# Performance work log

Hardware: AMD Instinct MI355X
Metric: run time of the kernel (lower is better)

Reference implementation:

```python
import jax, jax.numpy as jnp
import numpy as np

EPS = 1e-5
MAX_NORM = 1.0 - 1e-5  # clamp for atanh / ball projection


def mob_add(u, v):
    # Mobius addition on each d_ball (last dim), c=1
    uv = jnp.sum(u * v, axis=-1, keepdims=True)
    uu = jnp.sum(u * u, axis=-1, keepdims=True)
    vv = jnp.sum(v * v, axis=-1, keepdims=True)
    num = (1.0 + 2.0 * uv + vv) * u + (1.0 - uu) * v
    den = 1.0 + 2.0 * uv + uu * vv
    return num / jnp.maximum(den, EPS)


def log_map_zero(y):
    # log map at origin, per ball (last dim)
    n = jnp.linalg.norm(y, axis=-1, keepdims=True)
    n_c = jnp.clip(n, EPS, MAX_NORM)
    return jnp.arctanh(n_c) * y / n_c


def mob_mat_mul_d(W, x, d):
    # W: (n_in, d, n_out, d); x: (B, n_in, d) -> (B, n_out, d)
    # Mobius matvec on the flattened product-ball representation.
    B = x.shape[0]
    x_f = x.reshape(B, -1)                      # (B, n_in*d)
    W_f = W.reshape(x_f.shape[-1], -1)          # (n_in*d, n_out*d)
    Mx = x_f @ W_f                              # (B, n_out*d)
    x_n = jnp.clip(jnp.linalg.norm(x_f, axis=-1, keepdims=True), EPS, MAX_NORM)
    Mx_n = jnp.maximum(jnp.linalg.norm(Mx, axis=-1, keepdims=True), EPS)
    res = jnp.tanh(Mx_n / x_n * jnp.arctanh(x_n)) * (Mx / Mx_n)
    return res.reshape(B, -1, d)


def mob_pointwise_prod(x, u):
    # diagonal Mobius scaling of hyperbolic x by euclidean gate u, per ball
    ux = u * x
    x_n = jnp.clip(jnp.linalg.norm(x, axis=-1, keepdims=True), EPS, MAX_NORM)
    ux_n = jnp.maximum(jnp.linalg.norm(ux, axis=-1, keepdims=True), EPS)
    return jnp.tanh(ux_n / x_n * jnp.arctanh(x_n)) * (ux / ux_n)


def transition(W, h, U, x, b, d):
    Wh = mob_mat_mul_d(W, h, d)
    Ux = mob_mat_mul_d(U, x, d)
    return mob_add(mob_add(Wh, Ux), b)


def setup_inputs() -> dict:
    key = jax.random.key(0)
    ks = jax.random.split(key, 8)
    B, I, H, D = 16384, 256, 256, 4
    k = (1.0 / H) ** 0.5
    # scale points to lie strictly inside the Poincare ball
    hyp_x = 0.02 * jax.random.normal(ks[0], (B, I, D), dtype=jnp.float32)
    hidden = 0.02 * jax.random.normal(ks[1], (B, H, D), dtype=jnp.float32)
    mk = lambda kk, n_in: jax.random.uniform(kk, (n_in, D, H, D), minval=-k, maxval=k, dtype=jnp.float32)
    return dict(
        hyp_x=hyp_x, hidden=hidden,
        w_z=mk(ks[2], H), w_r=mk(ks[3], H), w_h=mk(ks[4], H),
        u_z=mk(ks[5], I), u_r=mk(ks[6], I), u_h=mk(ks[7], I),
        b_z=jnp.zeros((H, D), jnp.float32),
        b_r=jnp.zeros((H, D), jnp.float32),
        b_h=jnp.zeros((H, D), jnp.float32),
    )


def reference(hyp_x, hidden, w_z, w_r, w_h, u_z, u_r, u_h, b_z, b_r, b_h):
    d = hyp_x.shape[-1]
    z = jax.nn.sigmoid(log_map_zero(transition(w_z, hidden, u_z, hyp_x, b_z, d)))
    r = jax.nn.sigmoid(log_map_zero(transition(w_r, hidden, u_r, hyp_x, b_r, d)))
    r_point_h = mob_pointwise_prod(hidden, r)
    # NOTE: original code uses u_r here (not u_h) -- kept faithful
    h_tilde = transition(w_h, r_point_h, u_r, hyp_x, b_h, d)
    minus_h_oplus_htilde = mob_add(-hidden, h_tilde)
    new_h = mob_add(hidden, mob_pointwise_prod(minus_h_oplus_htilde, z))
    return new_h
```

## Files before the change

### kernel.cpp

```cpp
#include <hip/hip_runtime.h>
#include <stdint.h>

#define EPSF 1e-5f
#define MAXNF (1.0f - 1e-5f)

typedef __attribute__((ext_vector_type(8))) short short8;
typedef __attribute__((ext_vector_type(4))) float floatx4;

__device__ __forceinline__ unsigned short f2bf(float f){
  union { float f; uint32_t u; } v; v.f = f;
  return (unsigned short)((v.u + 0x7FFFu + ((v.u >> 16) & 1u)) >> 16);
}
__device__ __forceinline__ float bf2f(unsigned short s){
  union { uint32_t u; float f; } v; v.u = ((uint32_t)s) << 16;
  return v.f;
}
__device__ __forceinline__ float4 bf2f4(ushort4 s){
  return make_float4(bf2f(s.x), bf2f(s.y), bf2f(s.z), bf2f(s.w));
}
__device__ __forceinline__ uint32_t cvtpk(float lo, float hi){
  uint32_t r; asm("v_cvt_pk_bf16_f32 %0, %1, %2" : "=v"(r) : "v"(lo), "v"(hi));
  return r;
}
__device__ __forceinline__ void store_bf4(unsigned short* p, float4 v){
  uint2 r; r.x = cvtpk(v.x, v.y); r.y = cvtpk(v.z, v.w);
  *(uint2*)p = r;
}
__device__ __forceinline__ float fsqrt(float x){ return __builtin_amdgcn_sqrtf(x); }

__device__ __forceinline__ void gload16(const void* g, void* l){
  __builtin_amdgcn_global_load_lds(
      (__attribute__((address_space(1))) void*)(uintptr_t)g,
      (__attribute__((address_space(3))) void*)l, 16, 0, 0);
}

__device__ __forceinline__ float fatanh(float x){
  return 0.5f * __logf(__fdividef(1.f + x, 1.f - x));
}
__device__ __forceinline__ float ftanh_pos(float x){
  const float t = __expf(-2.f * x);
  return __fdividef(1.f - t, 1.f + t);
}
__device__ __forceinline__ float fsig(float x){
  return __fdividef(1.f, 1.f + __expf(-x));
}

__global__ __launch_bounds__(256, 4) void cast_norm_k(const float* __restrict__ X,
                                                      unsigned short* __restrict__ Xbf,
                                                      float* __restrict__ nrm){
  const int row = blockIdx.x, t = threadIdx.x;
  const float4 v = ((const float4*)(X + (size_t)row*1024))[t];
  store_bf4(Xbf + (size_t)row*1024 + 4*t, v);
  float ss = v.x*v.x + v.y*v.y + v.z*v.z + v.w*v.w;
  #pragma unroll
  for (int o = 32; o; o >>= 1) ss += __shfl_down(ss, o);
  __shared__ float red[4];
  const int lane = t & 63, w = t >> 6;
  if (lane == 0) red[w] = ss;
  __syncthreads();
  if (t == 0) nrm[row] = fsqrt(red[0] + red[1] + red[2] + red[3]);
}

__global__ void wcast_k(const float* __restrict__ W, unsigned short* __restrict__ Wt){
  __shared__ float tile[32][33];
  const int tx = threadIdx.x, ty = threadIdx.y;
  const int k0 = blockIdx.x * 32, n0 = blockIdx.y * 32;
  #pragma unroll
  for (int i = 0; i < 4; ++i)
    tile[ty + i*8][tx] = W[(size_t)(k0 + ty + i*8) * 1024 + n0 + tx];
  __syncthreads();
  #pragma unroll
  for (int i = 0; i < 4; ++i)
    Wt[(size_t)(n0 + ty + i*8) * 1024 + k0 + tx] = f2bf(tile[tx][ty + i*8]);
}

#define GBM 128
#define GBN 256
#define GBK 32
#define GKD 1024

__global__ __launch_bounds__(512) void gemm_k(const unsigned short* __restrict__ A,
                                              const unsigned short* __restrict__ Bt,
                                              unsigned short* __restrict__ C,
                                              int lda, int ldc){
  __shared__ unsigned short smem[2*4096 + 2*8192];
  unsigned short* As = smem;
  unsigned short* Bs = smem + 2*4096;
  const int tid = threadIdx.x;
  const int lane = tid & 63, w = tid >> 6;
  const int wr = w >> 2, wc = w & 3;
  const int lr = lane & 15, kg = lane >> 4;
  const int row0 = blockIdx.y * GBM, col0 = blockIdx.x * GBN;

  int aoff[4], boff[4];
  #pragma unroll
  for (int a = 0; a < 4; ++a){
    const int r = wr*64 + a*16 + lr;
    aoff[a] = r*32 + ((kg ^ (r & 3)) << 3);
  }
  #pragma unroll
  for (int b = 0; b < 4; ++b){
    const int r = wc*64 + b*16 + lr;
    boff[b] = r*32 + ((kg ^ (r & 3)) << 3);
  }

  floatx4 acc[4][4] = {};

  auto stage = [&](int buf, int kt){
    {
      const int flat = tid;
      const int r = flat >> 2, cp = flat & 3, c = cp ^ (r & 3);
      gload16(A + (size_t)(row0 + r)*lda + kt*GBK + c*8, As + buf*4096 + flat*8);
    }
    #pragma unroll
    for (int i = 0; i < 2; ++i){
      const int flat = i*512 + tid;
      const int r = flat >> 2, cp = flat & 3, c = cp ^ (r & 3);
      gload16(Bt + (size_t)(col0 + r)*GKD + kt*GBK + c*8, Bs + buf*8192 + flat*8);
    }
  };

  stage(0, 0);
  __syncthreads();
  int cur = 0;
  for (int kt = 0; kt < GKD/GBK; ++kt){
    if (kt + 1 < GKD/GBK) stage(cur ^ 1, kt + 1);
    const unsigned short* as = As + cur*4096;
    const unsigned short* bs = Bs + cur*8192;
    short8 af[4], bfv[4];
    #pragma unroll
    for (int a = 0; a < 4; ++a) af[a] = *(const short8*)(as + aoff[a]);
    #pragma unroll
    for (int b = 0; b < 4; ++b) bfv[b] = *(const short8*)(bs + boff[b]);
    #pragma unroll
    for (int a = 0; a < 4; ++a)
      #pragma unroll
      for (int b = 0; b < 4; ++b)
        acc[a][b] = __builtin_amdgcn_mfma_f32_16x16x32_bf16(af[a], bfv[b], acc[a][b], 0, 0, 0);
    __syncthreads();
    cur ^= 1;
  }

  const int crow0 = row0 + wr*64;
  const int ccol = col0 + wc*64 + lr;
  #pragma unroll
  for (int a = 0; a < 4; ++a){
    #pragma unroll
    for (int j = 0; j < 4; ++j){
      const int r = crow0 + a*16 + kg*4 + j;
      unsigned short* cp = C + (size_t)r*ldc + ccol;
      #pragma unroll
      for (int b = 0; b < 4; ++b) cp[b*16] = f2bf(acc[a][b][j]);
    }
  }
}

__device__ __forceinline__ float dot4(const float4 a, const float4 b){
  return a.x*b.x + a.y*b.y + a.z*b.z + a.w*b.w;
}
__device__ __forceinline__ float4 scal4(const float4 a, float s){
  return make_float4(a.x*s, a.y*s, a.z*s, a.w*s);
}
__device__ __forceinline__ float clipn(float n){ return fminf(fmaxf(n, EPSF), MAXNF); }

__device__ __forceinline__ float4 mob_add4(const float4 u, const float4 v){
  const float uv = dot4(u,v), uu = dot4(u,u), vv = dot4(v,v);
  const float cu = 1.f + 2.f*uv + vv, cv = 1.f - uu;
  const float inv = __fdividef(1.f, fmaxf(1.f + 2.f*uv + uu*vv, EPSF));
  return make_float4((cu*u.x + cv*v.x)*inv, (cu*u.y + cv*v.y)*inv,
                     (cu*u.z + cv*v.z)*inv, (cu*u.w + cv*v.w)*inv);
}

__device__ __forceinline__ float4 logmap_sig4(const float4 y){
  const float n = fsqrt(dot4(y,y));
  const float nc = clipn(n);
  const float s = __fdividef(fatanh(nc), nc);
  return make_float4(fsig(s*y.x), fsig(s*y.y), fsig(s*y.z), fsig(s*y.w));
}

__device__ __forceinline__ float4 mob_pp4(const float4 x, const float4 u){
  const float4 ux = make_float4(u.x*x.x, u.y*x.y, u.z*x.z, u.w*x.w);
  const float xn = clipn(fsqrt(dot4(x,x)));
  const float uxn = fmaxf(fsqrt(dot4(ux,ux)), EPSF);
  const float s = __fdividef(ftanh_pos(__fdividef(uxn, xn) * fatanh(xn)), uxn);
  return scal4(ux, s);
}

__global__ __launch_bounds__(256, 4) void epi1_k(unsigned short* C1, unsigned short* C2,
                       const float* hidden, const float* bz, const float* br,
                       const float* h_nrm, const float* x_nrm, float* rph_nrm){
  const int row = blockIdx.x, t = threadIdx.x;
  const int lane = t & 63, w = t >> 6;
  const size_t b2 = (size_t)row*2048;
  const float4 mzh  = bf2f4(((const ushort4*)(C1 + b2))[t]);
  const float4 mrh4 = bf2f4(((const ushort4*)(C1 + b2))[256 + t]);
  const float4 mzx4 = bf2f4(((const ushort4*)(C2 + b2))[t]);
  const float4 mrx4 = bf2f4(((const ushort4*)(C2 + b2))[256 + t]);
  float s0 = dot4(mzh,mzh), s1 = dot4(mzx4,mzx4), s2 = dot4(mrh4,mrh4), s3 = dot4(mrx4,mrx4);
  #pragma unroll
  for (int o = 32; o; o >>= 1){
    s0 += __shfl_down(s0,o); s1 += __shfl_down(s1,o);
    s2 += __shfl_down(s2,o); s3 += __shfl_down(s3,o);
  }
  __shared__ float red[4][4];
  if (lane == 0){ red[w][0]=s0; red[w][1]=s1; red[w][2]=s2; red[w][3]=s3; }
  __syncthreads();
  const float nMzh = fmaxf(fsqrt(red[0][0]+red[1][0]+red[2][0]+red[3][0]), EPSF);
  const float nMzx = fmaxf(fsqrt(red[0][1]+red[1][1]+red[2][1]+red[3][1]), EPSF);
  const float nMrh = fmaxf(fsqrt(red[0][2]+red[1][2]+red[2][2]+red[3][2]), EPSF);
  const float nMrx = fmaxf(fsqrt(red[0][3]+red[1][3]+red[2][3]+red[3][3]), EPSF);
  const float hnc = clipn(h_nrm[row]), xnc = clipn(x_nrm[row]);
  const float atH = fatanh(hnc), atX = fatanh(xnc);
  const float swz = __fdividef(ftanh_pos(__fdividef(nMzh, hnc)*atH), nMzh);
  const float suz = __fdividef(ftanh_pos(__fdividef(nMzx, xnc)*atX), nMzx);
  const float swr = __fdividef(ftanh_pos(__fdividef(nMrh, hnc)*atH), nMrh);
  const float sur = __fdividef(ftanh_pos(__fdividef(nMrx, xnc)*atX), nMrx);
  const float4 bz4 = ((const float4*)bz)[t];
  const float4 br4 = ((const float4*)br)[t];
  const float4 z4 = logmap_sig4(mob_add4(mob_add4(scal4(mzh,swz), scal4(mzx4,suz)), bz4));
  const float4 UxR = scal4(mrx4, sur);
  const float4 r4 = logmap_sig4(mob_add4(mob_add4(scal4(mrh4,swr), UxR), br4));
  store_bf4(C1 + b2 + 4*t, z4);
  store_bf4(C1 + b2 + 1024 + 4*t, UxR);
  const float4 h4 = ((const float4*)(hidden + (size_t)row*1024))[t];
  const float4 rph = mob_pp4(h4, r4);
  store_bf4(C2 + b2 + 4*t, rph);
  float sr = dot4(rph, rph);
  #pragma unroll
  for (int o = 32; o; o >>= 1) sr += __shfl_down(sr,o);
  __syncthreads();
  if (lane == 0) red[w][0] = sr;
  __syncthreads();
  if (t == 0) rph_nrm[row] = fsqrt(red[0][0]+red[1][0]+red[2][0]+red[3][0]);
}

__global__ __launch_bounds__(256, 4) void epi2_k(const unsigned short* mh,
                       const unsigned short* C1,
                       const float* hidden, const float* bh,
                       const float* rph_nrm, float* __restrict__ out){
  const int row = blockIdx.x, t = threadIdx.x;
  const int lane = t & 63, w = t >> 6;
  const size_t base = (size_t)row*1024, b2 = (size_t)row*2048;
  const float4 mh4 = bf2f4(((const ushort4*)(mh + base))[t]);
  float ss = dot4(mh4, mh4);
  #pragma unroll
  for (int o = 32; o; o >>= 1) ss += __shfl_down(ss,o);
  __shared__ float red[4];
  if (lane == 0) red[w] = ss;
  __syncthreads();
  const float nMh = fmaxf(fsqrt(red[0]+red[1]+red[2]+red[3]), EPSF);
  const float rnc = clipn(rph_nrm[row]);
  const float swh = __fdividef(ftanh_pos(__fdividef(nMh, rnc)*fatanh(rnc)), nMh);
  const float4 WhH = scal4(mh4, swh);
  const float4 Ux4 = bf2f4(((const ushort4*)(C1 + b2))[256 + t]);
  const float4 bh4 = ((const float4*)bh)[t];
  const float4 ht = mob_add4(mob_add4(WhH, Ux4), bh4);
  const float4 h4 = ((const float4*)(hidden + base))[t];
  const float4 nh4 = make_float4(-h4.x, -h4.y, -h4.z, -h4.w);
  const float4 m4 = mob_add4(nh4, ht);
  const float4 z4 = bf2f4(((const ushort4*)(C1 + b2))[t]);
  const float4 p4 = mob_pp4(m4, z4);
  const float4 o4 = mob_add4(h4, p4);
  ((float4*)(out + base))[t] = o4;
}

extern "C" void kernel_launch(void* const* d_in, const int* in_sizes, int n_in,
                              void* d_out, int out_size, void* d_ws, size_t ws_size,
                              hipStream_t stream) {
  (void)in_sizes; (void)n_in; (void)out_size; (void)ws_size;
  const float* hyp_x  = (const float*)d_in[0];
  const float* hidden = (const float*)d_in[1];
  const float* w_z = (const float*)d_in[2];
  const float* w_r = (const float*)d_in[3];
  const float* w_h = (const float*)d_in[4];
  const float* u_z = (const float*)d_in[5];
  const float* u_r = (const float*)d_in[6];
  const float* b_z = (const float*)d_in[8];
  const float* b_r = (const float*)d_in[9];
  const float* b_h = (const float*)d_in[10];
  float* out = (float*)d_out;

  const size_t NROW = 16384, MAT = NROW*1024;
  unsigned short* hbf = (unsigned short*)d_ws;
  unsigned short* xbf = hbf + MAT;
  unsigned short* C1  = xbf + MAT;
  unsigned short* wzr = C1 + 2*MAT;
  unsigned short* uzr = wzr + 2*1048576;
  unsigned short* wht = uzr + 2*1048576;
  float* h_n   = (float*)(wht + 1048576);
  float* x_n   = h_n + NROW;
  float* rph_n = x_n + NROW;
  unsigned short* C2 = (unsigned short*)d_out;

  cast_norm_k<<<dim3(16384), dim3(256), 0, stream>>>(hidden, hbf, h_n);
  cast_norm_k<<<dim3(16384), dim3(256), 0, stream>>>(hyp_x, xbf, x_n);

  dim3 wg(32, 32), wb(32, 8);
  wcast_k<<<wg, wb, 0, stream>>>(w_z, wzr);
  wcast_k<<<wg, wb, 0, stream>>>(w_r, wzr + 1048576);
  wcast_k<<<wg, wb, 0, stream>>>(u_z, uzr);
  wcast_k<<<wg, wb, 0, stream>>>(u_r, uzr + 1048576);
  wcast_k<<<wg, wb, 0, stream>>>(w_h, wht);

  gemm_k<<<dim3(8,128), dim3(512), 0, stream>>>(hbf, wzr, C1, 1024, 2048);
  gemm_k<<<dim3(8,128), dim3(512), 0, stream>>>(xbf, uzr, C2, 1024, 2048);

  epi1_k<<<dim3(16384), dim3(256), 0, stream>>>(C1, C2, hidden, b_z, b_r,
                                                h_n, x_n, rph_n);

  gemm_k<<<dim3(4,128), dim3(512), 0, stream>>>(C2 , wht,
                                                hbf , 2048, 1024);

  epi2_k<<<dim3(16384), dim3(256), 0, stream>>>(hbf, C1, hidden, b_h, rph_n, out);
}
```

Baseline: 374.6 us.

## Map one row per wavefront in row kernels and read hidden from bf16 copy

The cast and epilogue kernels now process one row per 64-lane wavefront, four rows per block, using xor-shuffle reductions in place of shared-memory reductions and block barriers. The epilogues read the bf16 copy of hidden instead of the fp32 input, which halves that traffic at some precision cost. The third GEMM now writes into the spare half of C2 rather than overwriting hbf, so hbf stays valid for the second epilogue. The aim is to cut barrier and launch overhead and memory traffic in the bandwidth-bound elementwise stages, in exchange for lower-precision hidden values in the epilogue math.

Result: faster. 347.4 us (-7.2%).

```diff
diff --git a/kernel.cpp b/kernel.cpp
--- a/kernel.cpp
+++ b/kernel.cpp
@@ -11,22 +11,26 @@
   union { float f; uint32_t u; } v; v.f = f;
   return (unsigned short)((v.u + 0x7FFFu + ((v.u >> 16) & 1u)) >> 16);
 }
-__device__ __forceinline__ float bf2f(unsigned short s){
-  union { uint32_t u; float f; } v; v.u = ((uint32_t)s) << 16;
-  return v.f;
-}
-__device__ __forceinline__ float4 bf2f4(ushort4 s){
-  return make_float4(bf2f(s.x), bf2f(s.y), bf2f(s.z), bf2f(s.w));
+__device__ __forceinline__ float bf_lo(uint32_t u){
+  union { uint32_t u; float f; } v; v.u = u << 16; return v.f;
+}
+__device__ __forceinline__ float bf_hi(uint32_t u){
+  union { uint32_t u; float f; } v; v.u = u & 0xffff0000u; return v.f;
 }
 __device__ __forceinline__ uint32_t cvtpk(float lo, float hi){
   uint32_t r; asm("v_cvt_pk_bf16_f32 %0, %1, %2" : "=v"(r) : "v"(lo), "v"(hi));
   return r;
 }
-__device__ __forceinline__ void store_bf4(unsigned short* p, float4 v){
-  uint2 r; r.x = cvtpk(v.x, v.y); r.y = cvtpk(v.z, v.w);
-  *(uint2*)p = r;
-}
 __device__ __forceinline__ float fsqrt(float x){ return __builtin_amdgcn_sqrtf(x); }
+
+__device__ __forceinline__ float4 ld_ball(const unsigned short* rowp, int b){
+  const uint2 u = *(const uint2*)(rowp + 4*b);
+  return make_float4(bf_lo(u.x), bf_hi(u.x), bf_lo(u.y), bf_hi(u.y));
+}
+__device__ __forceinline__ void st_ball(unsigned short* rowp, int b, float4 f){
+  uint2 u; u.x = cvtpk(f.x, f.y); u.y = cvtpk(f.z, f.w);
+  *(uint2*)(rowp + 4*b) = u;
+}
 
 __device__ __forceinline__ void gload16(const void* g, void* l){
   __builtin_amdgcn_global_load_lds(
@@ -45,20 +49,56 @@
   return __fdividef(1.f, 1.f + __expf(-x));
 }
 
-__global__ __launch_bounds__(256, 4) void cast_norm_k(const float* __restrict__ X,
-                                                      unsigned short* __restrict__ Xbf,
-                                                      float* __restrict__ nrm){
-  const int row = blockIdx.x, t = threadIdx.x;
-  const float4 v = ((const float4*)(X + (size_t)row*1024))[t];
-  store_bf4(Xbf + (size_t)row*1024 + 4*t, v);
-  float ss = v.x*v.x + v.y*v.y + v.z*v.z + v.w*v.w;
-  #pragma unroll
-  for (int o = 32; o; o >>= 1) ss += __shfl_down(ss, o);
-  __shared__ float red[4];
-  const int lane = t & 63, w = t >> 6;
-  if (lane == 0) red[w] = ss;
-  __syncthreads();
-  if (t == 0) nrm[row] = fsqrt(red[0] + red[1] + red[2] + red[3]);
+__device__ __forceinline__ float wsum(float v){
+  #pragma unroll
+  for (int o = 32; o; o >>= 1) v += __shfl_xor(v, o);
+  return v;
+}
+
+__device__ __forceinline__ float dot4(const float4 a, const float4 b){
+  return a.x*b.x + a.y*b.y + a.z*b.z + a.w*b.w;
+}
+__device__ __forceinline__ float4 scal4(const float4 a, float s){
+  return make_float4(a.x*s, a.y*s, a.z*s, a.w*s);
+}
+__device__ __forceinline__ float clipn(float n){ return fminf(fmaxf(n, EPSF), MAXNF); }
+
+__device__ __forceinline__ float4 mob_add4(const float4 u, const float4 v){
+  const float uv = dot4(u,v), uu = dot4(u,u), vv = dot4(v,v);
+  const float cu = 1.f + 2.f*uv + vv, cv = 1.f - uu;
+  const float inv = __fdividef(1.f, fmaxf(1.f + 2.f*uv + uu*vv, EPSF));
+  return make_float4((cu*u.x + cv*v.x)*inv, (cu*u.y + cv*v.y)*inv,
+                     (cu*u.z + cv*v.z)*inv, (cu*u.w + cv*v.w)*inv);
+}
+__device__ __forceinline__ float4 logmap_sig4(const float4 y){
+  const float nc = clipn(fsqrt(dot4(y,y)));
+  const float s = __fdividef(fatanh(nc), nc);
+  return make_float4(fsig(s*y.x), fsig(s*y.y), fsig(s*y.z), fsig(s*y.w));
+}
+__device__ __forceinline__ float4 mob_pp4(const float4 x, const float4 u){
+  const float4 ux = make_float4(u.x*x.x, u.y*x.y, u.z*x.z, u.w*x.w);
+  const float xn = clipn(fsqrt(dot4(x,x)));
+  const float uxn = fmaxf(fsqrt(dot4(ux,ux)), EPSF);
+  const float s = __fdividef(ftanh_pos(__fdividef(uxn, xn) * fatanh(xn)), uxn);
+  return scal4(ux, s);
+}
+
+__global__ void cast_norm_k(const float* __restrict__ X, unsigned short* __restrict__ Xbf,
+                            float* __restrict__ nrm){
+  const int lane = threadIdx.x & 63;
+  const int row  = blockIdx.x*4 + (threadIdx.x >> 6);
+  const float4* xr = (const float4*)(X + (size_t)row*1024);
+  unsigned short* br_ = Xbf + (size_t)row*1024;
+  float ss = 0.f;
+  #pragma unroll
+  for (int i = 0; i < 4; ++i){
+    const int b = lane + 64*i;
+    const float4 v = xr[b];
+    st_ball(br_, b, v);
+    ss += dot4(v, v);
+  }
+  ss = wsum(ss);
+  if (lane == 0) nrm[row] = fsqrt(ss);
 }
 
 __global__ void wcast_k(const float* __restrict__ W, unsigned short* __restrict__ Wt){
@@ -155,113 +195,99 @@
   }
 }
 
-__device__ __forceinline__ float dot4(const float4 a, const float4 b){
-  return a.x*b.x + a.y*b.y + a.z*b.z + a.w*b.w;
-}
-__device__ __forceinline__ float4 scal4(const float4 a, float s){
-  return make_float4(a.x*s, a.y*s, a.z*s, a.w*s);
-}
-__device__ __forceinline__ float clipn(float n){ return fminf(fmaxf(n, EPSF), MAXNF); }
-
-__device__ __forceinline__ float4 mob_add4(const float4 u, const float4 v){
-  const float uv = dot4(u,v), uu = dot4(u,u), vv = dot4(v,v);
-  const float cu = 1.f + 2.f*uv + vv, cv = 1.f - uu;
-  const float inv = __fdividef(1.f, fmaxf(1.f + 2.f*uv + uu*vv, EPSF));
-  return make_float4((cu*u.x + cv*v.x)*inv, (cu*u.y + cv*v.y)*inv,
-                     (cu*u.z + cv*v.z)*inv, (cu*u.w + cv*v.w)*inv);
-}
-
-__device__ __forceinline__ float4 logmap_sig4(const float4 y){
-  const float n = fsqrt(dot4(y,y));
-  const float nc = clipn(n);
-  const float s = __fdividef(fatanh(nc), nc);
-  return make_float4(fsig(s*y.x), fsig(s*y.y), fsig(s*y.z), fsig(s*y.w));
-}
-
-__device__ __forceinline__ float4 mob_pp4(const float4 x, const float4 u){
-  const float4 ux = make_float4(u.x*x.x, u.y*x.y, u.z*x.z, u.w*x.w);
-  const float xn = clipn(fsqrt(dot4(x,x)));
-  const float uxn = fmaxf(fsqrt(dot4(ux,ux)), EPSF);
-  const float s = __fdividef(ftanh_pos(__fdividef(uxn, xn) * fatanh(xn)), uxn);
-  return scal4(ux, s);
-}
-
-__global__ __launch_bounds__(256, 4) void epi1_k(unsigned short* C1, unsigned short* C2,
-                       const float* hidden, const float* bz, const float* br,
-                       const float* h_nrm, const float* x_nrm, float* rph_nrm){
-  const int row = blockIdx.x, t = threadIdx.x;
-  const int lane = t & 63, w = t >> 6;
-  const size_t b2 = (size_t)row*2048;
-  const float4 mzh  = bf2f4(((const ushort4*)(C1 + b2))[t]);
-  const float4 mrh4 = bf2f4(((const ushort4*)(C1 + b2))[256 + t]);
-  const float4 mzx4 = bf2f4(((const ushort4*)(C2 + b2))[t]);
-  const float4 mrx4 = bf2f4(((const ushort4*)(C2 + b2))[256 + t]);
-  float s0 = dot4(mzh,mzh), s1 = dot4(mzx4,mzx4), s2 = dot4(mrh4,mrh4), s3 = dot4(mrx4,mrx4);
-  #pragma unroll
-  for (int o = 32; o; o >>= 1){
-    s0 += __shfl_down(s0,o); s1 += __shfl_down(s1,o);
-    s2 += __shfl_down(s2,o); s3 += __shfl_down(s3,o);
-  }
-  __shared__ float red[4][4];
-  if (lane == 0){ red[w][0]=s0; red[w][1]=s1; red[w][2]=s2; red[w][3]=s3; }
-  __syncthreads();
-  const float nMzh = fmaxf(fsqrt(red[0][0]+red[1][0]+red[2][0]+red[3][0]), EPSF);
-  const float nMzx = fmaxf(fsqrt(red[0][1]+red[1][1]+red[2][1]+red[3][1]), EPSF);
-  const float nMrh = fmaxf(fsqrt(red[0][2]+red[1][2]+red[2][2]+red[3][2]), EPSF);
-  const float nMrx = fmaxf(fsqrt(red[0][3]+red[1][3]+red[2][3]+red[3][3]), EPSF);
+__global__ __launch_bounds__(256) __attribute__((amdgpu_waves_per_eu(4,4)))
+void epi1_k(unsigned short* C1, unsigned short* C2, const unsigned short* hbf,
+            const float* bz, const float* br,
+            const float* h_nrm, const float* x_nrm, float* rph_nrm){
+  const int lane = threadIdx.x & 63;
+  const int row  = blockIdx.x*4 + (threadIdx.x >> 6);
+  unsigned short* c1lo = C1 + (size_t)row*2048;
+  unsigned short* c1hi = c1lo + 1024;
+  unsigned short* c2lo = C2 + (size_t)row*2048;
+  unsigned short* c2hi = c2lo + 1024;
+  const unsigned short* hr = hbf + (size_t)row*1024;
+
+  float4 mzh[4], mrh[4], mzx[4], mrx[4];
+  float s0 = 0.f, s1 = 0.f, s2 = 0.f, s3 = 0.f;
+  #pragma unroll
+  for (int i = 0; i < 4; ++i){
+    const int b = lane + 64*i;
+    mzh[i] = ld_ball(c1lo, b); mrh[i] = ld_ball(c1hi, b);
+    mzx[i] = ld_ball(c2lo, b); mrx[i] = ld_ball(c2hi, b);
+    s0 += dot4(mzh[i], mzh[i]); s1 += dot4(mzx[i], mzx[i]);
+    s2 += dot4(mrh[i], mrh[i]); s3 += dot4(mrx[i], mrx[i]);
+  }
+  s0 = wsum(s0); s1 = wsum(s1); s2 = wsum(s2); s3 = wsum(s3);
+
+  const float nMzh = fmaxf(fsqrt(s0), EPSF);
+  const float nMzx = fmaxf(fsqrt(s1), EPSF);
+  const float nMrh = fmaxf(fsqrt(s2), EPSF);
+  const float nMrx = fmaxf(fsqrt(s3), EPSF);
   const float hnc = clipn(h_nrm[row]), xnc = clipn(x_nrm[row]);
   const float atH = fatanh(hnc), atX = fatanh(xnc);
   const float swz = __fdividef(ftanh_pos(__fdividef(nMzh, hnc)*atH), nMzh);
   const float suz = __fdividef(ftanh_pos(__fdividef(nMzx, xnc)*atX), nMzx);
   const float swr = __fdividef(ftanh_pos(__fdividef(nMrh, hnc)*atH), nMrh);
   const float sur = __fdividef(ftanh_pos(__fdividef(nMrx, xnc)*atX), nMrx);
-  const float4 bz4 = ((const float4*)bz)[t];
-  const float4 br4 = ((const float4*)br)[t];
-  const float4 z4 = logmap_sig4(mob_add4(mob_add4(scal4(mzh,swz), scal4(mzx4,suz)), bz4));
-  const float4 UxR = scal4(mrx4, sur);
-  const float4 r4 = logmap_sig4(mob_add4(mob_add4(scal4(mrh4,swr), UxR), br4));
-  store_bf4(C1 + b2 + 4*t, z4);
-  store_bf4(C1 + b2 + 1024 + 4*t, UxR);
-  const float4 h4 = ((const float4*)(hidden + (size_t)row*1024))[t];
-  const float4 rph = mob_pp4(h4, r4);
-  store_bf4(C2 + b2 + 4*t, rph);
-  float sr = dot4(rph, rph);
-  #pragma unroll
-  for (int o = 32; o; o >>= 1) sr += __shfl_down(sr,o);
-  __syncthreads();
-  if (lane == 0) red[w][0] = sr;
-  __syncthreads();
-  if (t == 0) rph_nrm[row] = fsqrt(red[0][0]+red[1][0]+red[2][0]+red[3][0]);
-}
-
-__global__ __launch_bounds__(256, 4) void epi2_k(const unsigned short* mh,
-                       const unsigned short* C1,
-                       const float* hidden, const float* bh,
-                       const float* rph_nrm, float* __restrict__ out){
-  const int row = blockIdx.x, t = threadIdx.x;
-  const int lane = t & 63, w = t >> 6;
-  const size_t base = (size_t)row*1024, b2 = (size_t)row*2048;
-  const float4 mh4 = bf2f4(((const ushort4*)(mh + base))[t]);
-  float ss = dot4(mh4, mh4);
-  #pragma unroll
-  for (int o = 32; o; o >>= 1) ss += __shfl_down(ss,o);
-  __shared__ float red[4];
-  if (lane == 0) red[w] = ss;
-  __syncthreads();
-  const float nMh = fmaxf(fsqrt(red[0]+red[1]+red[2]+red[3]), EPSF);
+
+  float sr = 0.f;
+  #pragma unroll
+  for (int i = 0; i < 4; ++i){
+    const int b = lane + 64*i;
+    const float4 bz4 = ((const float4*)bz)[b];
+    const float4 br4 = ((const float4*)br)[b];
+    const float4 z4  = logmap_sig4(mob_add4(mob_add4(scal4(mzh[i],swz), scal4(mzx[i],suz)), bz4));
+    const float4 UxR = scal4(mrx[i], sur);
+    const float4 r4  = logmap_sig4(mob_add4(mob_add4(scal4(mrh[i],swr), UxR), br4));
+    st_ball(c1lo, b, z4);
+    st_ball(c1hi, b, UxR);
+    const float4 h4  = ld_ball(hr, b);
+    const float4 rph = mob_pp4(h4, r4);
+    st_ball(c2lo, b, rph);
+    sr += dot4(rph, rph);
+  }
+  sr = wsum(sr);
+  if (lane == 0) rph_nrm[row] = fsqrt(sr);
+}
+
+__global__ __launch_bounds__(256) __attribute__((amdgpu_waves_per_eu(4,4)))
+void epi2_k(const unsigned short* C1, const unsigned short* C2,
+            const unsigned short* hbf, const float* bh,
+            const float* rph_nrm, float* out){
+  const int lane = threadIdx.x & 63;
+  const int row  = blockIdx.x*4 + (threadIdx.x >> 6);
+  const unsigned short* c1lo = C1 + (size_t)row*2048;
+  const unsigned short* c1hi = c1lo + 1024;
+  const unsigned short* c2hi = C2 + (size_t)row*2048 + 1024;
+  const unsigned short* hr = hbf + (size_t)row*1024;
+  float4* outr = (float4*)(out + (size_t)row*1024);
+
+  float4 mh[4];
+  float ss = 0.f;
+  #pragma unroll
+  for (int i = 0; i < 4; ++i){
+    mh[i] = ld_ball(c2hi, lane + 64*i);
+    ss += dot4(mh[i], mh[i]);
+  }
+  ss = wsum(ss);
+  const float nMh = fmaxf(fsqrt(ss), EPSF);
   const float rnc = clipn(rph_nrm[row]);
   const float swh = __fdividef(ftanh_pos(__fdividef(nMh, rnc)*fatanh(rnc)), nMh);
-  const float4 WhH = scal4(mh4, swh);
-  const float4 Ux4 = bf2f4(((const ushort4*)(C1 + b2))[256 + t]);
-  const float4 bh4 = ((const float4*)bh)[t];
-  const float4 ht = mob_add4(mob_add4(WhH, Ux4), bh4);
-  const float4 h4 = ((const float4*)(hidden + base))[t];
-  const float4 nh4 = make_float4(-h4.x, -h4.y, -h4.z, -h4.w);
-  const float4 m4 = mob_add4(nh4, ht);
-  const float4 z4 = bf2f4(((const ushort4*)(C1 + b2))[t]);
-  const float4 p4 = mob_pp4(m4, z4);
-  const float4 o4 = mob_add4(h4, p4);
-  ((float4*)(out + base))[t] = o4;
+
+  #pragma unroll
+  for (int i = 0; i < 4; ++i){
+    const int b = lane + 64*i;
+    const float4 WhH = scal4(mh[i], swh);
+    const float4 Ux4 = ld_ball(c1hi, b);
+    const float4 bh4 = ((const float4*)bh)[b];
+    const float4 ht  = mob_add4(mob_add4(WhH, Ux4), bh4);
+    const float4 h4  = ld_ball(hr, b);
+    const float4 nh4 = make_float4(-h4.x, -h4.y, -h4.z, -h4.w);
+    const float4 m4  = mob_add4(nh4, ht);
+    const float4 z4  = ld_ball(c1lo, b);
+    const float4 p4  = mob_pp4(m4, z4);
+    outr[b] = mob_add4(h4, p4);
+  }
 }
 
 extern "C" void kernel_launch(void* const* d_in, const int* in_sizes, int n_in,
@@ -292,8 +318,8 @@
   float* rph_n = x_n + NROW;
   unsigned short* C2 = (unsigned short*)d_out;
 
-  cast_norm_k<<<dim3(16384), dim3(256), 0, stream>>>(hidden, hbf, h_n);
-  cast_norm_k<<<dim3(16384), dim3(256), 0, stream>>>(hyp_x, xbf, x_n);
+  cast_norm_k<<<dim3(4096), dim3(256), 0, stream>>>(hidden, hbf, h_n);
+  cast_norm_k<<<dim3(4096), dim3(256), 0, stream>>>(hyp_x, xbf, x_n);
 
   dim3 wg(32, 32), wb(32, 8);
   wcast_k<<<wg, wb, 0, stream>>>(w_z, wzr);
@@ -305,11 +331,9 @@
   gemm_k<<<dim3(8,128), dim3(512), 0, stream>>>(hbf, wzr, C1, 1024, 2048);
   gemm_k<<<dim3(8,128), dim3(512), 0, stream>>>(xbf, uzr, C2, 1024, 2048);
 
-  epi1_k<<<dim3(16384), dim3(256), 0, stream>>>(C1, C2, hidden, b_z, b_r,
-                                                h_n, x_n, rph_n);
-
-  gemm_k<<<dim3(4,128), dim3(512), 0, stream>>>(C2 , wht,
-                                                hbf , 2048, 1024);
-
-  epi2_k<<<dim3(16384), dim3(256), 0, stream>>>(hbf, C1, hidden, b_h, rph_n, out);
-}
+  epi1_k<<<dim3(4096), dim3(256), 0, stream>>>(C1, C2, hbf, b_z, b_r, h_n, x_n, rph_n);
+
+  gemm_k<<<dim3(4,128), dim3(512), 0, stream>>>(C2, wht, C2 + 1024, 2048, 2048);
+
+  epi2_k<<<dim3(4096), dim3(256), 0, stream>>>(C1, C2, hbf, b_h, rph_n, out);
+}
```
